# Kernel optimization log

Hardware: AMD Instinct MI355X
Metric: run time of the kernel (lower is better)

The kernel has to match this reference:

```python
import jax, jax.numpy as jnp
import numpy as np

B, N_BINS, D, G = 2048, 200, 128, 100  # batch, bins (MTL_token_num), feature dim, genes per bin


def setup_inputs() -> dict:
    key = jax.random.key(0)
    k_x, k_w = jax.random.split(key)
    MTL_tokens = jax.random.normal(k_x, (B, N_BINS, D), dtype=jnp.float32)
    # Xavier-uniform init per head: bound = sqrt(6 / (fan_in + fan_out))
    bound = float(np.sqrt(6.0 / (D + G)))
    W = jax.random.uniform(k_w, (N_BINS, G, D), dtype=jnp.float32, minval=-bound, maxval=bound)
    b = jnp.zeros((N_BINS, G), dtype=jnp.float32)
    return {"MTL_tokens": MTL_tokens, "W": W, "b": b}


def reference(MTL_tokens, W, b):
    # Original: for each bin idx, head_idx(MTL_tokens[:, idx]) -> [B, G], collected as a list
    # of length N_BINS, then every scalar is unpacked in (bin, batch, gene) order.
    # Batched grouped GEMM over bins: [B,N,D] x [N,G,D] -> [N,B,G]
    y = jnp.einsum('bnd,ngd->nbg', MTL_tokens, W) + b[:, None, :]
    # activation is None in this config; flatten in (bin, batch, gene) order == the
    # scalar-unpacking double loop of the original module.
    return y.reshape(-1)
```

## Files before the change

### kernel.cpp

```cpp
#include <hip/hip_runtime.h>
#include <hip/hip_bf16.h>

#define NB    200
#define BSZ   2048
#define DD    128
#define GG    100
#define WROWS 112
#define ROWB  256
#define WIMG  (WROWS * ROWB)
#define NTILE (NB * 16)
#define NBLK  512

typedef __attribute__((ext_vector_type(8))) short  short8;
typedef __attribute__((ext_vector_type(4))) float  f32x4;
typedef __attribute__((ext_vector_type(4))) int    i32x4;

__device__ __forceinline__ unsigned f2bf_pack(float lo, float hi) {
    unsigned ulo = __builtin_bit_cast(unsigned, lo);
    ulo += 0x7FFFu + ((ulo >> 16) & 1u);
    unsigned uhi = __builtin_bit_cast(unsigned, hi);
    uhi += 0x7FFFu + ((uhi >> 16) & 1u);
    return (ulo >> 16) | (uhi & 0xFFFF0000u);
}

__device__ __forceinline__ void gload_lds16(const void* g, void* l) {
    __builtin_amdgcn_global_load_lds(
        (const __attribute__((address_space(1))) unsigned int*)g,
        (__attribute__((address_space(3))) unsigned int*)l, 16, 0, 0);
}

#define WAIT_LGKM0() do { asm volatile("" ::: "memory");     \
                          __builtin_amdgcn_s_waitcnt(0xC07F);\
                          __builtin_amdgcn_sched_barrier(0); \
                          __builtin_amdgcn_wave_barrier();   \
                          asm volatile("" ::: "memory"); } while (0)

#define BARRIER_LGKM() do { asm volatile("" ::: "memory");      \
                            __builtin_amdgcn_s_waitcnt(0xC07F); \
                            __builtin_amdgcn_s_barrier();       \
                            __builtin_amdgcn_sched_barrier(0);  \
                            asm volatile("" ::: "memory"); } while (0)

#define BARRIER_VM14() do { asm volatile("s_waitcnt vmcnt(14)" ::: "memory"); \
                            __builtin_amdgcn_s_barrier();        \
                            __builtin_amdgcn_sched_barrier(0);   \
                            asm volatile("" ::: "memory"); } while (0)

#define BARRIER_VM0() do { asm volatile("s_waitcnt vmcnt(0) lgkmcnt(0)" ::: "memory"); \
                           __builtin_amdgcn_s_barrier();        \
                           __builtin_amdgcn_sched_barrier(0);   \
                           asm volatile("" ::: "memory"); } while (0)


__global__ __launch_bounds__(256) void wconv_kernel(
    const float* __restrict__ W, unsigned char* __restrict__ ws)
{
    const int gidx = blockIdx.x * 256 + threadIdx.x;
    if (gidx >= NB * WROWS * 16) return;
    const int gr  = gidx & 15;
    const int row = (gidx >> 4) % WROWS;
    const int n   = gidx / (WROWS * 16);
    i32x4 pack = (i32x4){0, 0, 0, 0};
    if (row < GG) {
        const float* src = W + ((size_t)n * GG + row) * DD + gr * 8;
        const f32x4 a = *reinterpret_cast<const f32x4*>(src);
        const f32x4 b = *reinterpret_cast<const f32x4*>(src + 4);
        pack.x = (int)f2bf_pack(a[0], a[1]);
        pack.y = (int)f2bf_pack(a[2], a[3]);
        pack.z = (int)f2bf_pack(b[0], b[1]);
        pack.w = (int)f2bf_pack(b[2], b[3]);
    }
    const int off = row * ROWB + ((gr * 16) ^ ((row & 7) << 4));
    *reinterpret_cast<i32x4*>(ws + (size_t)n * WIMG + off) = pack;
}

__device__ __forceinline__ void stage_tile(char* buf, const unsigned char* WS,
                                           int n, int lane, int wid) {
    const unsigned char* src = WS + (size_t)n * WIMG;
    #pragma unroll
    for (int i = 0; i < 7; ++i) {
        const int c = i * 4 + wid;
        gload_lds16(src + c * 1024 + lane * 16, buf + c * 1024);
    }
}

__device__ __forceinline__ void load_x(f32x4 (&raw)[2][4][2], const float* X,
                                       int tile, int wid, int l15, int lhi) {
    const int n = tile >> 4;
    const int rowbase = (tile & 15) * 128 + wid * 32;
    #pragma unroll
    for (int rf = 0; rf < 2; ++rf) {
        const float* xrow = X + ((size_t)(rowbase + rf * 16 + l15) * NB + n) * DD + lhi * 8;
        #pragma unroll
        for (int ks = 0; ks < 4; ++ks) {
            raw[rf][ks][0] = *reinterpret_cast<const f32x4*>(xrow + ks * 32);
            raw[rf][ks][1] = *reinterpret_cast<const f32x4*>(xrow + ks * 32 + 4);
        }
    }
}

__device__ __forceinline__ void conv_x(const f32x4 (&raw)[2][4][2],
                                       short8 (&areg)[2][4]) {
    #pragma unroll
    for (int rf = 0; rf < 2; ++rf)
        #pragma unroll
        for (int ks = 0; ks < 4; ++ks) {
            const f32x4 a = raw[rf][ks][0];
            const f32x4 b = raw[rf][ks][1];
            i32x4 pk;
            pk.x = (int)f2bf_pack(a[0], a[1]);
            pk.y = (int)f2bf_pack(a[2], a[3]);
            pk.z = (int)f2bf_pack(b[0], b[1]);
            pk.w = (int)f2bf_pack(b[2], b[3]);
            areg[rf][ks] = __builtin_bit_cast(short8, pk);
        }
}

__global__ __launch_bounds__(256, 2) void mtl_heads_runs(
    const float* __restrict__ X, const float* __restrict__ Bias,
    const unsigned char* __restrict__ WS, float* __restrict__ Out)
{
    const int tid  = threadIdx.x;
    const int lane = tid & 63;
    const int wid  = tid >> 6;
    const int l15  = lane & 15;
    const int lhi  = lane >> 4;

    __shared__ __align__(16) char smem[2 * WIMG];
    char* wbuf = smem;
    char* obuf = smem + WIMG;

    const int s   = ((blockIdx.x & 7) << 6) + (blockIdx.x >> 3);
    const int cnt = ((s & 3) == 0) ? 7 : 6;
    int t = 6 * s + ((s + 3) >> 2);

    stage_tile(wbuf, WS, t >> 4, lane, wid);
    f32x4 raw[2][4][2];
    load_x(raw, X, t, wid, l15, lhi);
    BARRIER_VM0();
    short8 areg[2][4];
    conv_x(raw, areg);

    for (int i = 0; i < cnt; ++i, ++t) {
        const int  n       = t >> 4;
        const int  rowbase = (t & 15) * 128 + wid * 32;
        const bool hasnext = (i + 1 < cnt);
        const bool binchg  = hasnext && (((t + 1) & 15) == 0);

        if (binchg)  stage_tile(obuf, WS, (t + 1) >> 4, lane, wid);
        if (hasnext) load_x(raw, X, t + 1, wid, l15, lhi);
        float bias[7];
        #pragma unroll
        for (int cf = 0; cf < 7; ++cf) {
            const int g = cf * 16 + l15;
            bias[cf] = (g < GG) ? Bias[n * GG + g] : 0.0f;
        }

        f32x4 acc[2][7];
        #pragma unroll
        for (int rf = 0; rf < 2; ++rf)
            #pragma unroll
            for (int cf = 0; cf < 7; ++cf)
                acc[rf][cf] = (f32x4){0.f, 0.f, 0.f, 0.f};

        #pragma unroll
        for (int cf = 0; cf < 7; ++cf) {
            const int g    = cf * 16 + l15;
            const int rowb = g * ROWB;
            const int swz  = (g & 7) << 4;
            #pragma unroll
            for (int ks = 0; ks < 4; ++ks) {
                const int off = rowb + (((lhi * 16) + ks * 64) ^ swz);
                const i32x4 braw = *reinterpret_cast<const i32x4*>(wbuf + off);
                const short8 bfrag = __builtin_bit_cast(short8, braw);
                acc[0][cf] = __builtin_amdgcn_mfma_f32_16x16x32_bf16(areg[0][ks], bfrag, acc[0][cf], 0, 0, 0);
                acc[1][cf] = __builtin_amdgcn_mfma_f32_16x16x32_bf16(areg[1][ks], bfrag, acc[1][cf], 0, 0, 0);
            }
        }

        BARRIER_LGKM();

        char* scratch = (binchg ? wbuf : obuf) + wid * 6400;
        float* lds_f = reinterpret_cast<float*>(scratch);
        #pragma unroll
        for (int rf = 0; rf < 2; ++rf) {
            #pragma unroll
            for (int cf = 0; cf < 7; ++cf) {
                const int g = cf * 16 + l15;
                if (g < GG) {
                    #pragma unroll
                    for (int j = 0; j < 4; ++j)
                        lds_f[(lhi * 4 + j) * GG + g] = acc[rf][cf][j] + bias[cf];
                }
            }
            WAIT_LGKM0();
            char* dst = (char*)(Out + ((size_t)n * BSZ + rowbase + rf * 16) * GG);
            #pragma unroll
            for (int it = 0; it < 7; ++it) {
                const int c = it * 64 + lane;
                if (c < 400) {
                    const i32x4 v = *reinterpret_cast<const i32x4*>(scratch + c * 16);
                    __builtin_nontemporal_store(v, reinterpret_cast<i32x4*>(dst + c * 16));
                }
            }
            WAIT_LGKM0();
        }

        if (hasnext) conv_x(raw, areg);

        BARRIER_VM14();

        if (binchg) { char* tmp = wbuf; wbuf = obuf; obuf = tmp; }
    }
}

__global__ __launch_bounds__(256, 4) void mtl_heads_fallback(
    const float* __restrict__ X, const float* __restrict__ W,
    const float* __restrict__ Bias, float* __restrict__ Out)
{
    const int n     = blockIdx.y;
    const int mtile = blockIdx.x;
    const int tid   = threadIdx.x;
    const int lane  = tid & 63;
    const int wid   = tid >> 6;
    const int l15   = lane & 15;
    const int lhi   = lane >> 4;

    __shared__ __align__(16) char smem[WIMG];

    {
        const int rsub = tid >> 4;
        const int k0   = (tid & 15) * 8;
        #pragma unroll
        for (int it = 0; it < 7; ++it) {
            const int row = it * 16 + rsub;
            i32x4 pack = (i32x4){0, 0, 0, 0};
            if (row < GG) {
                const float* s = W + ((size_t)n * GG + row) * DD + k0;
                const f32x4 a = *reinterpret_cast<const f32x4*>(s);
                const f32x4 b = *reinterpret_cast<const f32x4*>(s + 4);
                pack.x = (int)f2bf_pack(a[0], a[1]);
                pack.y = (int)f2bf_pack(a[2], a[3]);
                pack.z = (int)f2bf_pack(b[0], b[1]);
                pack.w = (int)f2bf_pack(b[2], b[3]);
            }
            const int off = row * ROWB + ((k0 * 2) ^ ((row & 7) << 4));
            *reinterpret_cast<i32x4*>(smem + off) = pack;
        }
    }

    const int rowbase = mtile * 128 + wid * 32;
    f32x4 raw[2][4][2];
    load_x(raw, X, n * 16 + mtile, wid, l15, lhi);
    float bias[7];
    #pragma unroll
    for (int cf = 0; cf < 7; ++cf) {
        const int g = cf * 16 + l15;
        bias[cf] = (g < GG) ? Bias[n * GG + g] : 0.0f;
    }
    short8 areg[2][4];
    conv_x(raw, areg);

    __syncthreads();

    f32x4 acc[2][7];
    #pragma unroll
    for (int rf = 0; rf < 2; ++rf)
        #pragma unroll
        for (int cf = 0; cf < 7; ++cf)
            acc[rf][cf] = (f32x4){0.f, 0.f, 0.f, 0.f};

    #pragma unroll
    for (int cf = 0; cf < 7; ++cf) {
        const int g    = cf * 16 + l15;
        const int rowb = g * ROWB;
        const int swz  = (g & 7) << 4;
        #pragma unroll
        for (int ks = 0; ks < 4; ++ks) {
            const int off = rowb + (((lhi * 16) + ks * 64) ^ swz);
            const i32x4 braw = *reinterpret_cast<const i32x4*>(smem + off);
            const short8 bfrag = __builtin_bit_cast(short8, braw);
            acc[0][cf] = __builtin_amdgcn_mfma_f32_16x16x32_bf16(areg[0][ks], bfrag, acc[0][cf], 0, 0, 0);
            acc[1][cf] = __builtin_amdgcn_mfma_f32_16x16x32_bf16(areg[1][ks], bfrag, acc[1][cf], 0, 0, 0);
        }
    }

    __syncthreads();

    float* lds_f = reinterpret_cast<float*>(smem + wid * 6400);
    #pragma unroll
    for (int rf = 0; rf < 2; ++rf) {
        #pragma unroll
        for (int cf = 0; cf < 7; ++cf) {
            const int g = cf * 16 + l15;
            if (g < GG) {
                #pragma unroll
                for (int j = 0; j < 4; ++j)
                    lds_f[(lhi * 4 + j) * GG + g] = acc[rf][cf][j] + bias[cf];
            }
        }
        WAIT_LGKM0();
        const char* rgn = smem + wid * 6400;
        char* dst = (char*)(Out + ((size_t)n * BSZ + rowbase + rf * 16) * GG);
        #pragma unroll
        for (int it = 0; it < 7; ++it) {
            const int c = it * 64 + lane;
            if (c < 400) {
                const i32x4 v = *reinterpret_cast<const i32x4*>(rgn + c * 16);
                *reinterpret_cast<i32x4*>(dst + c * 16) = v;
            }
        }
        WAIT_LGKM0();
    }
}

extern "C" void kernel_launch(void* const* d_in, const int* in_sizes, int n_in,
                              void* d_out, int out_size, void* d_ws, size_t ws_size,
                              hipStream_t stream) {
    (void)in_sizes; (void)n_in; (void)out_size;
    const float* X    = (const float*)d_in[0];
    const float* W    = (const float*)d_in[1];
    const float* Bias = (const float*)d_in[2];
    float* Out        = (float*)d_out;
    const size_t wsneed = (size_t)NB * WIMG;
    if (ws_size >= wsneed) {
        wconv_kernel<<<(NB * WROWS * 16 + 255) / 256, 256, 0, stream>>>(W, (unsigned char*)d_ws);
        mtl_heads_runs<<<dim3(NBLK), 256, 0, stream>>>(X, Bias, (const unsigned char*)d_ws, Out);
    } else {
        mtl_heads_fallback<<<dim3(16, NB), 256, 0, stream>>>(X, W, Bias, Out);
    }
}
```

Before: 72.46 us.

## Give each wave private LDS scratch and barrier only on bin change

```diff
diff --git a/kernel.cpp b/kernel.cpp
--- a/kernel.cpp
+++ b/kernel.cpp
@@ -8,6 +8,8 @@
 #define WROWS 112
 #define ROWB  256
 #define WIMG  (WROWS * ROWB)
+#define WLDS  (GG * ROWB)
+#define SCR   6400
 #define NTILE (NB * 16)
 #define NBLK  512
 
@@ -35,16 +37,10 @@
                           __builtin_amdgcn_wave_barrier();   \
                           asm volatile("" ::: "memory"); } while (0)
 
-#define BARRIER_LGKM() do { asm volatile("" ::: "memory");      \
-                            __builtin_amdgcn_s_waitcnt(0xC07F); \
-                            __builtin_amdgcn_s_barrier();       \
-                            __builtin_amdgcn_sched_barrier(0);  \
-                            asm volatile("" ::: "memory"); } while (0)
-
-#define BARRIER_VM14() do { asm volatile("s_waitcnt vmcnt(14)" ::: "memory"); \
-                            __builtin_amdgcn_s_barrier();        \
-                            __builtin_amdgcn_sched_barrier(0);   \
-                            asm volatile("" ::: "memory"); } while (0)
+#define BARRIER_STAGE() do { asm volatile("s_waitcnt vmcnt(14)" ::: "memory"); \
+                             __builtin_amdgcn_s_barrier();        \
+                             __builtin_amdgcn_sched_barrier(0);   \
+                             asm volatile("" ::: "memory"); } while (0)
 
 #define BARRIER_VM0() do { asm volatile("s_waitcnt vmcnt(0) lgkmcnt(0)" ::: "memory"); \
                            __builtin_amdgcn_s_barrier();        \
@@ -78,10 +74,12 @@
                                            int n, int lane, int wid) {
     const unsigned char* src = WS + (size_t)n * WIMG;
     #pragma unroll
-    for (int i = 0; i < 7; ++i) {
+    for (int i = 0; i < 6; ++i) {
         const int c = i * 4 + wid;
         gload_lds16(src + c * 1024 + lane * 16, buf + c * 1024);
     }
+    if (wid == 0)
+        gload_lds16(src + 24 * 1024 + lane * 16, buf + 24 * 1024);
 }
 
 __device__ __forceinline__ void load_x(f32x4 (&raw)[2][4][2], const float* X,
@@ -116,7 +114,7 @@
         }
 }
 
-__global__ __launch_bounds__(256, 2) void mtl_heads_runs(
+__global__ __launch_bounds__(256, 2) void mtl_heads_free(
     const float* __restrict__ X, const float* __restrict__ Bias,
     const unsigned char* __restrict__ WS, float* __restrict__ Out)
 {
@@ -126,9 +124,10 @@
     const int l15  = lane & 15;
     const int lhi  = lane >> 4;
 
-    __shared__ __align__(16) char smem[2 * WIMG];
+    __shared__ __align__(16) char smem[2 * WLDS + 4 * SCR];
     char* wbuf = smem;
-    char* obuf = smem + WIMG;
+    char* obuf = smem + WLDS;
+    char* scratch = smem + 2 * WLDS + wid * SCR;
 
     const int s   = ((blockIdx.x & 7) << 6) + (blockIdx.x >> 3);
     const int cnt = ((s & 3) == 0) ? 7 : 6;
@@ -178,12 +177,9 @@
             }
         }
 
-        BARRIER_LGKM();
-
-        char* scratch = (binchg ? wbuf : obuf) + wid * 6400;
-        float* lds_f = reinterpret_cast<float*>(scratch);
         #pragma unroll
         for (int rf = 0; rf < 2; ++rf) {
+            float* lds_f = reinterpret_cast<float*>(scratch);
             #pragma unroll
             for (int cf = 0; cf < 7; ++cf) {
                 const int g = cf * 16 + l15;
@@ -208,9 +204,10 @@
 
         if (hasnext) conv_x(raw, areg);
 
-        BARRIER_VM14();
-
-        if (binchg) { char* tmp = wbuf; wbuf = obuf; obuf = tmp; }
+        if (binchg) {
+            BARRIER_STAGE();
+            char* tmp = wbuf; wbuf = obuf; obuf = tmp;
+        }
     }
 }
 
@@ -236,9 +233,9 @@
             const int row = it * 16 + rsub;
             i32x4 pack = (i32x4){0, 0, 0, 0};
             if (row < GG) {
-                const float* s = W + ((size_t)n * GG + row) * DD + k0;
-                const f32x4 a = *reinterpret_cast<const f32x4*>(s);
-                const f32x4 b = *reinterpret_cast<const f32x4*>(s + 4);
+                const float* sp = W + ((size_t)n * GG + row) * DD + k0;
+                const f32x4 a = *reinterpret_cast<const f32x4*>(sp);
+                const f32x4 b = *reinterpret_cast<const f32x4*>(sp + 4);
                 pack.x = (int)f2bf_pack(a[0], a[1]);
                 pack.y = (int)f2bf_pack(a[2], a[3]);
                 pack.z = (int)f2bf_pack(b[0], b[1]);
@@ -287,7 +284,7 @@
 
     __syncthreads();
 
-    float* lds_f = reinterpret_cast<float*>(smem + wid * 6400);
+    float* lds_f = reinterpret_cast<float*>(smem + wid * SCR);
     #pragma unroll
     for (int rf = 0; rf < 2; ++rf) {
         #pragma unroll
@@ -300,7 +297,7 @@
             }
         }
         WAIT_LGKM0();
-        const char* rgn = smem + wid * 6400;
+        const char* rgn = smem + wid * SCR;
         char* dst = (char*)(Out + ((size_t)n * BSZ + rowbase + rf * 16) * GG);
         #pragma unroll
         for (int it = 0; it < 7; ++it) {
@@ -325,7 +322,7 @@
     const size_t wsneed = (size_t)NB * WIMG;
     if (ws_size >= wsneed) {
         wconv_kernel<<<(NB * WROWS * 16 + 255) / 256, 256, 0, stream>>>(W, (unsigned char*)d_ws);
-        mtl_heads_runs<<<dim3(NBLK), 256, 0, stream>>>(X, Bias, (const unsigned char*)d_ws, Out);
+        mtl_heads_free<<<dim3(NBLK), 256, 0, stream>>>(X, Bias, (const unsigned char*)d_ws, Out);
     } else {
         mtl_heads_fallback<<<dim3(16, NB), 256, 0, stream>>>(X, W, Bias, Out);
     }
```

Measured after the change: 71.92 us. No clear change (-0.7%).
